# Optimization experiments

Hardware: AMD Instinct MI355X
Metric: run time of the kernel (lower is better)

The kernel has to match this reference:

```python
import jax, jax.numpy as jnp
import numpy as np
from jax import lax

B, C, H, W = 16, 32, 384, 384
NK = 32          # num_kernels == out_channels (group_size forced to 1)
K = 3            # kernel_size
HID = 128        # kernel_generator hidden width


def setup_inputs() -> dict:
    key = jax.random.key(0)
    ks = jax.random.split(key, 5)
    x  = jax.random.normal(ks[0], (B, C, H, W), dtype=jnp.float32)
    # torch.nn.Linear weights stored transposed for y = x @ w + b
    w1 = jax.random.normal(ks[1], (C, HID), dtype=jnp.float32) * (1.0 / np.sqrt(C))
    b1 = jnp.zeros((HID,), dtype=jnp.float32)
    w2 = jax.random.normal(ks[2], (HID, NK * K * K), dtype=jnp.float32) * (1.0 / np.sqrt(HID))
    b2 = jnp.zeros((NK * K * K,), dtype=jnp.float32)
    return {"x": x, "w1": w1, "b1": b1, "w2": w2, "b2": b2}


def reference(x, w1, b1, w2, b2):
    b, c, h, w = x.shape
    # kernel generator: global avg pool -> MLP -> per-sample depthwise kernels
    pooled = x.mean(axis=(2, 3))                         # [B, C]
    hdn = jax.nn.relu(pooled @ w1 + b1)                  # [B, 128]
    kernels = (hdn @ w2 + b2).reshape(b, NK, K, K)       # [B, NK, K, K]
    # per-sample dynamic depthwise conv: fold batch into channel groups
    xg = x[:, :NK].reshape(1, b * NK, h, w)              # [1, B*NK, H, W]
    wgt = kernels.reshape(b * NK, 1, K, K)               # [B*NK, 1, K, K]
    pad = K // 2
    out = lax.conv_general_dilated(
        xg, wgt,
        window_strides=(1, 1),
        padding=[(pad, pad), (pad, pad)],
        feature_group_count=b * NK,
        dimension_numbers=("NCHW", "OIHW", "NCHW"),
    )
    return out.reshape(b, NK, h, w)
```

## Files before the change

kernel.cpp:

```cpp
#include <hip/hip_runtime.h>

#define BB   16
#define CC   32
#define HH   384
#define WW   384
#define HW   (HH * WW)
#define HID  128
#define KOUT 288
#define NPLANE (BB * CC)

#define SAMPLES_PER_CHUNK 8
#define NCHUNK (BB / SAMPLES_PER_CHUNK)
#define PLANES_PER_CHUNK (SAMPLES_PER_CHUNK * CC)

#define CG_PER_ROW 96
#define ROWS_PER_THREAD 24
#define NBANDS (HH / ROWS_PER_THREAD)
#define THREADS_PER_PLANE (CG_PER_ROW * NBANDS)
#define BLOCKS_PER_PLANE (THREADS_PER_PLANE / 256)

typedef float f4 __attribute__((ext_vector_type(4)));

__global__ __launch_bounds__(1024) void pool_kernel(const float* __restrict__ x,
                                                    float* __restrict__ pooled,
                                                    int plane_base) {
    const int bc = plane_base + blockIdx.x;
    const f4* pv = (const f4*)(x + (size_t)bc * HW);
    float s = 0.f;
    for (int i = threadIdx.x; i < HW / 4; i += 1024) {
        f4 v = pv[i];
        s += (v.x + v.y) + (v.z + v.w);
    }
#pragma unroll
    for (int off = 32; off; off >>= 1) s += __shfl_down(s, off);
    __shared__ float red[16];
    if ((threadIdx.x & 63) == 0) red[threadIdx.x >> 6] = s;
    __syncthreads();
    if (threadIdx.x == 0) {
        float t = 0.f;
#pragma unroll
        for (int wv = 0; wv < 16; ++wv) t += red[wv];
        pooled[bc] = t * (1.0f / (float)HW);
    }
}

__global__ __launch_bounds__(128) void mlp_kernel(const float* __restrict__ pooled,
                                                  const float* __restrict__ w1,
                                                  const float* __restrict__ b1,
                                                  const float* __restrict__ w2,
                                                  const float* __restrict__ b2,
                                                  float* __restrict__ kern,
                                                  int sample_base) {
    const int b   = sample_base + blockIdx.x;
    const int tid = threadIdx.x;
    __shared__ float pc[CC];
    __shared__ float hdn[HID];
    if (tid < CC) pc[tid] = pooled[b * CC + tid];
    __syncthreads();

    float a = b1[tid];
#pragma unroll
    for (int c = 0; c < CC; ++c) a += pc[c] * w1[c * HID + tid];
    hdn[tid] = fmaxf(a, 0.f);
    __syncthreads();

    for (int o = tid; o < KOUT; o += 128) {
        float a2 = b2[o];
#pragma unroll 8
        for (int j = 0; j < HID; ++j) a2 += hdn[j] * w2[j * KOUT + o];
        kern[b * KOUT + o] = a2;
    }
}

__device__ __forceinline__ void load_row6(const float* __restrict__ xp,
                                          int r, int c0, int cg, float* a) {
    if ((unsigned)r < (unsigned)HH) {
        const float* p = xp + r * WW + c0;
        const f4 v = *reinterpret_cast<const f4*>(p);
        a[0] = (cg > 0)              ? p[-1] : 0.f;
        a[1] = v.x; a[2] = v.y; a[3] = v.z; a[4] = v.w;
        a[5] = (cg < CG_PER_ROW - 1) ? p[4]  : 0.f;
    } else {
        a[0] = a[1] = a[2] = a[3] = a[4] = a[5] = 0.f;
    }
}

__global__ __launch_bounds__(256) void conv_kernel(const float* __restrict__ x,
                                                   const float* __restrict__ kern,
                                                   float* __restrict__ out,
                                                   int plane_base) {
    const int plane = plane_base + (int)(blockIdx.x / BLOCKS_PER_PLANE);
    const int rem   = (blockIdx.x % BLOCKS_PER_PLANE) * 256 + (int)threadIdx.x;
    const int band  = rem / CG_PER_ROW;
    const int cg    = rem - band * CG_PER_ROW;
    const int c0    = cg * 4;

    const float* xp = x   + (size_t)plane * HW;
    float*       op = out + (size_t)plane * HW;

    float w[9];
    const float* kw = kern + plane * 9;
#pragma unroll
    for (int t = 0; t < 9; ++t) w[t] = kw[t];

    const int r0 = band * ROWS_PER_THREAD;
    float aT[6], aM[6], aB[6];
    float aN[6] = {0.f, 0.f, 0.f, 0.f, 0.f, 0.f};
    load_row6(xp, r0 - 1, c0, cg, aT);
    load_row6(xp, r0,     c0, cg, aM);
    load_row6(xp, r0 + 1, c0, cg, aB);

#pragma unroll
    for (int i = 0; i < ROWS_PER_THREAD; ++i) {
        const int r = r0 + i;
        if (i < ROWS_PER_THREAD - 1)
            load_row6(xp, r + 2, c0, cg, aN);

        f4 o;
        o.x = w[0]*aT[0] + w[1]*aT[1] + w[2]*aT[2]
            + w[3]*aM[0] + w[4]*aM[1] + w[5]*aM[2]
            + w[6]*aB[0] + w[7]*aB[1] + w[8]*aB[2];
        o.y = w[0]*aT[1] + w[1]*aT[2] + w[2]*aT[3]
            + w[3]*aM[1] + w[4]*aM[2] + w[5]*aM[3]
            + w[6]*aB[1] + w[7]*aB[2] + w[8]*aB[3];
        o.z = w[0]*aT[2] + w[1]*aT[3] + w[2]*aT[4]
            + w[3]*aM[2] + w[4]*aM[3] + w[5]*aM[4]
            + w[6]*aB[2] + w[7]*aB[3] + w[8]*aB[4];
        o.w = w[0]*aT[3] + w[1]*aT[4] + w[2]*aT[5]
            + w[3]*aM[3] + w[4]*aM[4] + w[5]*aM[5]
            + w[6]*aB[3] + w[7]*aB[4] + w[8]*aB[5];

        __builtin_nontemporal_store(o, reinterpret_cast<f4*>(op + (size_t)r * WW + c0));

#pragma unroll
        for (int t = 0; t < 6; ++t) { aT[t] = aM[t]; aM[t] = aB[t]; aB[t] = aN[t]; }
    }
}

extern "C" void kernel_launch(void* const* d_in, const int* in_sizes, int n_in,
                              void* d_out, int out_size, void* d_ws, size_t ws_size,
                              hipStream_t stream) {
    const float* x  = (const float*)d_in[0];
    const float* w1 = (const float*)d_in[1];
    const float* b1 = (const float*)d_in[2];
    const float* w2 = (const float*)d_in[3];
    const float* b2 = (const float*)d_in[4];
    float* out = (float*)d_out;

    float* pooled = (float*)d_ws;
    float* kern   = pooled + BB * CC;

    for (int ch = 0; ch < NCHUNK; ++ch) {
        const int pbase = ch * PLANES_PER_CHUNK;
        const int sbase = ch * SAMPLES_PER_CHUNK;
        pool_kernel<<<PLANES_PER_CHUNK, 1024, 0, stream>>>(x, pooled, pbase);
        mlp_kernel<<<SAMPLES_PER_CHUNK, 128, 0, stream>>>(pooled, w1, b1, w2, b2, kern, sbase);
        conv_kernel<<<PLANES_PER_CHUNK * BLOCKS_PER_PLANE, 256, 0, stream>>>(x, kern, out, pbase);
    }
}
```

Measured before the change: 600.5 us.

## Fuse kernel-generator MLP into conv kernel and shrink chunk size

Removes the separate MLP launch: every conv block recomputes the hidden layer and its own 9 kernel weights from the pooled means in shared memory, with a shuffle reduction for the second layer. The first input rows are loaded before the MLP so the loads can overlap the weight computation. The chunk size drops from 8 to 4 samples, giving more but smaller pool/conv launches, presumably so more of each chunk's x stays in cache between pooling and convolution. The cost is redundant MLP work in every block, extra barriers, and more launches.

```diff
diff --git a/kernel.cpp b/kernel.cpp
--- a/kernel.cpp
+++ b/kernel.cpp
@@ -9,7 +9,7 @@
 #define KOUT 288
 #define NPLANE (BB * CC)
 
-#define SAMPLES_PER_CHUNK 8
+#define SAMPLES_PER_CHUNK 4
 #define NCHUNK (BB / SAMPLES_PER_CHUNK)
 #define PLANES_PER_CHUNK (SAMPLES_PER_CHUNK * CC)
 
@@ -44,34 +44,6 @@
     }
 }
 
-__global__ __launch_bounds__(128) void mlp_kernel(const float* __restrict__ pooled,
-                                                  const float* __restrict__ w1,
-                                                  const float* __restrict__ b1,
-                                                  const float* __restrict__ w2,
-                                                  const float* __restrict__ b2,
-                                                  float* __restrict__ kern,
-                                                  int sample_base) {
-    const int b   = sample_base + blockIdx.x;
-    const int tid = threadIdx.x;
-    __shared__ float pc[CC];
-    __shared__ float hdn[HID];
-    if (tid < CC) pc[tid] = pooled[b * CC + tid];
-    __syncthreads();
-
-    float a = b1[tid];
-#pragma unroll
-    for (int c = 0; c < CC; ++c) a += pc[c] * w1[c * HID + tid];
-    hdn[tid] = fmaxf(a, 0.f);
-    __syncthreads();
-
-    for (int o = tid; o < KOUT; o += 128) {
-        float a2 = b2[o];
-#pragma unroll 8
-        for (int j = 0; j < HID; ++j) a2 += hdn[j] * w2[j * KOUT + o];
-        kern[b * KOUT + o] = a2;
-    }
-}
-
 __device__ __forceinline__ void load_row6(const float* __restrict__ xp,
                                           int r, int c0, int cg, float* a) {
     if ((unsigned)r < (unsigned)HH) {
@@ -86,30 +58,62 @@
 }
 
 __global__ __launch_bounds__(256) void conv_kernel(const float* __restrict__ x,
-                                                   const float* __restrict__ kern,
+                                                   const float* __restrict__ pooled,
+                                                   const float* __restrict__ w1,
+                                                   const float* __restrict__ b1,
+                                                   const float* __restrict__ w2,
+                                                   const float* __restrict__ b2,
                                                    float* __restrict__ out,
                                                    int plane_base) {
     const int plane = plane_base + (int)(blockIdx.x / BLOCKS_PER_PLANE);
+    const int bs    = plane >> 5;
+    const int chn   = plane & 31;
     const int rem   = (blockIdx.x % BLOCKS_PER_PLANE) * 256 + (int)threadIdx.x;
     const int band  = rem / CG_PER_ROW;
     const int cg    = rem - band * CG_PER_ROW;
     const int c0    = cg * 4;
+    const int tid   = threadIdx.x;
 
     const float* xp = x   + (size_t)plane * HW;
     float*       op = out + (size_t)plane * HW;
+    const int r0 = band * ROWS_PER_THREAD;
 
-    float w[9];
-    const float* kw = kern + plane * 9;
-#pragma unroll
-    for (int t = 0; t < 9; ++t) w[t] = kw[t];
-
-    const int r0 = band * ROWS_PER_THREAD;
     float aT[6], aM[6], aB[6];
-    float aN[6] = {0.f, 0.f, 0.f, 0.f, 0.f, 0.f};
     load_row6(xp, r0 - 1, c0, cg, aT);
     load_row6(xp, r0,     c0, cg, aM);
     load_row6(xp, r0 + 1, c0, cg, aB);
 
+    __shared__ float pc_s[CC];
+    __shared__ float hdn_s[HID];
+    __shared__ float wsh[9];
+    if (tid < CC) pc_s[tid] = pooled[bs * CC + tid];
+    __syncthreads();
+    if (tid < HID) {
+        float a = b1[tid];
+#pragma unroll
+        for (int c = 0; c < CC; ++c) a += pc_s[c] * w1[c * HID + tid];
+        hdn_s[tid] = fmaxf(a, 0.f);
+    }
+    __syncthreads();
+    if (tid < 144) {
+        const int o  = tid >> 4;
+        const int j0 = (tid & 15) * 8;
+        const int oc = chn * 9 + o;
+        float a2 = 0.f;
+#pragma unroll
+        for (int j = 0; j < 8; ++j) a2 += hdn_s[j0 + j] * w2[(j0 + j) * KOUT + oc];
+        a2 += __shfl_down(a2, 8);
+        a2 += __shfl_down(a2, 4);
+        a2 += __shfl_down(a2, 2);
+        a2 += __shfl_down(a2, 1);
+        if ((tid & 15) == 0) wsh[o] = a2 + b2[oc];
+    }
+    __syncthreads();
+    float w[9];
+#pragma unroll
+    for (int t = 0; t < 9; ++t) w[t] = wsh[t];
+
+    float aN[6] = {0.f, 0.f, 0.f, 0.f, 0.f, 0.f};
 #pragma unroll
     for (int i = 0; i < ROWS_PER_THREAD; ++i) {
         const int r = r0 + i;
@@ -148,13 +152,11 @@
     float* out = (float*)d_out;
 
     float* pooled = (float*)d_ws;
-    float* kern   = pooled + BB * CC;
 
     for (int ch = 0; ch < NCHUNK; ++ch) {
         const int pbase = ch * PLANES_PER_CHUNK;
-        const int sbase = ch * SAMPLES_PER_CHUNK;
         pool_kernel<<<PLANES_PER_CHUNK, 1024, 0, stream>>>(x, pooled, pbase);
-        mlp_kernel<<<SAMPLES_PER_CHUNK, 128, 0, stream>>>(pooled, w1, b1, w2, b2, kern, sbase);
-        conv_kernel<<<PLANES_PER_CHUNK * BLOCKS_PER_PLANE, 256, 0, stream>>>(x, kern, out, pbase);
+        conv_kernel<<<PLANES_PER_CHUNK * BLOCKS_PER_PLANE, 256, 0, stream>>>(
+            x, pooled, w1, b1, w2, b2, out, pbase);
     }
 }
```

Result: faster. 577.3 us (-3.9%).
